# Performance work log

Measured on AMD Instinct MI355X. Metric: run time of the kernel, lower is better.

## Reference

```python
import jax, jax.numpy as jnp
import numpy as np

B, T, D, H, NH = 128, 64, 64, 128, 4


def setup_inputs() -> dict:
    key = jax.random.key(0)
    ks = jax.random.split(key, 32)
    s = 0.05
    inp = {
        "x": jax.random.normal(ks[0], (B, T, D), dtype=jnp.float32),
        "mask": jnp.ones((B, T), dtype=jnp.int32),
        # per-feature GRU params (input size 1, PyTorch gate order r,z,n)
        "Wih": jax.random.normal(ks[1], (D, 3 * H), dtype=jnp.float32) * s,
        "Whh": jax.random.normal(ks[2], (D, 3 * H, H), dtype=jnp.float32) * s,
        "bih": jax.random.normal(ks[3], (D, 3 * H), dtype=jnp.float32) * s,
        "bhh": jax.random.normal(ks[4], (D, 3 * H), dtype=jnp.float32) * s,
        # MHA projections (stored [in,out]; y = x @ W + b)
        "Wq": jax.random.normal(ks[5], (H, H), dtype=jnp.float32) * s,
        "bq": jnp.zeros((H,), dtype=jnp.float32),
        "Wk": jax.random.normal(ks[6], (H, H), dtype=jnp.float32) * s,
        "bk": jnp.zeros((H,), dtype=jnp.float32),
        "Wv": jax.random.normal(ks[7], (H, H), dtype=jnp.float32) * s,
        "bv": jnp.zeros((H,), dtype=jnp.float32),
        "Wo": jax.random.normal(ks[8], (H, H), dtype=jnp.float32) * s,
        "bo": jnp.zeros((H,), dtype=jnp.float32),
        # FFN
        "W1": jax.random.normal(ks[9], (H, 2 * H), dtype=jnp.float32) * s,
        "b1": jnp.zeros((2 * H,), dtype=jnp.float32),
        "W2": jax.random.normal(ks[10], (2 * H, H), dtype=jnp.float32) * s,
        "b2": jnp.zeros((H,), dtype=jnp.float32),
        # LayerNorms
        "g1": jnp.ones((H,), dtype=jnp.float32),
        "be1": jnp.zeros((H,), dtype=jnp.float32),
        "g2": jnp.ones((H,), dtype=jnp.float32),
        "be2": jnp.zeros((H,), dtype=jnp.float32),
        # FinalAttentionQKV
        "Fq": jax.random.normal(ks[11], (H, H), dtype=jnp.float32) * s,
        "fbq": jnp.zeros((H,), dtype=jnp.float32),
        "Fk": jax.random.normal(ks[12], (H, H), dtype=jnp.float32) * s,
        "fbk": jnp.zeros((H,), dtype=jnp.float32),
        "Fv": jax.random.normal(ks[13], (H, H), dtype=jnp.float32) * s,
        "fbv": jnp.zeros((H,), dtype=jnp.float32),
        "Fout": jax.random.normal(ks[14], (H,), dtype=jnp.float32) * s,
        "fbout": jnp.zeros((), dtype=jnp.float32),
    }
    return inp


def _layernorm(x, g, b, eps=1e-5):
    m = jnp.mean(x, axis=-1, keepdims=True)
    v = jnp.mean((x - m) ** 2, axis=-1, keepdims=True)
    return (x - m) * jax.lax.rsqrt(v + eps) * g + b


def _forward(x, mask, Wih, Whh, bih, bhh, Wq, bq, Wk, bk, Wv, bv, Wo, bo,
             W1, b1, W2, b2, g1, be1, g2, be2,
             Fq, fbq, Fk, fbk, Fv, fbv, Fout, fbout):
    Bc, Tc, Dc = x.shape
    Hc = Whh.shape[-1]

    # --- D independent GRUs, fused: batch axes (B, D), scalar input per step ---
    def step(h, xt):  # h: [B,D,H], xt: [B,D]
        gx = xt[..., None] * Wih + bih                     # [B,D,3H]
        gh = jnp.einsum('bdh,dkh->bdk', h, Whh) + bhh      # [B,D,3H]
        r = jax.nn.sigmoid(gx[..., :Hc] + gh[..., :Hc])
        z = jax.nn.sigmoid(gx[..., Hc:2 * Hc] + gh[..., Hc:2 * Hc])
        n = jnp.tanh(gx[..., 2 * Hc:] + r * gh[..., 2 * Hc:])
        hn = (1.0 - z) * n + z * h
        return hn, hn

    xs = jnp.transpose(x, (1, 0, 2))                        # [T,B,D]
    h0 = jnp.zeros((Bc, Dc, Hc), dtype=x.dtype)
    _, ys = jax.lax.scan(step, h0, xs)                      # [T,B,D,H]

    # last_by_lengths: gather hidden state at index lengths-1 per batch element
    lengths = jnp.sum(mask, axis=1)                         # [B]
    idx = jnp.clip(lengths - 1, 0, Tc - 1)
    emb = ys[idx, jnp.arange(Bc)]                           # [B,D,H] (D tokens)

    # --- MHA (self-attention over D feature tokens); dropout = identity (eval) ---
    dk = Hc // NH
    def split_heads(t):
        return jnp.transpose(t.reshape(Bc, Dc, NH, dk), (0, 2, 1, 3))  # [B,NH,D,dk]
    q = split_heads(emb @ Wq + bq)
    k = split_heads(emb @ Wk + bk)
    v = split_heads(emb @ Wv + bv)
    scores = jnp.einsum('bhnd,bhmd->bhnm', q, k) / jnp.sqrt(jnp.float32(dk))
    attn = jax.nn.softmax(scores, axis=-1)
    o = jnp.einsum('bhnm,bhmd->bhnd', attn, v)
    o = jnp.transpose(o, (0, 2, 1, 3)).reshape(Bc, Dc, Hc)
    mha_out = o @ Wo + bo

    h1 = _layernorm(emb + mha_out, g1, be1)
    ffn = jax.nn.relu(h1 @ W1 + b1) @ W2 + b2
    h2 = _layernorm(h1 + ffn, g2, be2)

    # --- FinalAttentionQKV ---
    fq = (h2[:, -1, :] @ Fq + fbq)[:, None, :]              # [B,1,H]
    fk = h2 @ Fk + fbk                                      # [B,D,H]
    fv = h2 @ Fv + fbv                                      # [B,D,H]
    e = jnp.tanh(fq + fk) @ Fout + fbout                    # [B,D]
    a = jax.nn.softmax(e, axis=-1)
    return jnp.einsum('bn,bnh->bh', a, fv)                  # [B,H]


def reference(x, mask, Wih, Whh, bih, bhh, Wq, bq, Wk, bk, Wv, bv, Wo, bo,
              W1, b1, W2, b2, g1, be1, g2, be2,
              Fq, fbq, Fk, fbk, Fv, fbv, Fout, fbout):
    return _forward(x, mask, Wih, Whh, bih, bhh, Wq, bq, Wk, bk, Wv, bv, Wo, bo,
                    W1, b1, W2, b2, g1, be1, g2, be2,
                    Fq, fbq, Fk, fbk, Fv, fbv, Fout, fbout)
```

## Files before the change

kernel.cpp:

```cpp
#include <hip/hip_runtime.h>
#include <hip/hip_bf16.h>
#include <math.h>

#define BB 128
#define TT 64
#define DD 64
#define HH 128
#define NHH 4
#define K3H 384

typedef __attribute__((ext_vector_type(8))) short short8_t;
typedef __attribute__((ext_vector_type(4))) float float4_t;

#define LOG2E 1.4426950408889634f

__device__ __forceinline__ unsigned short f2bf(float f) {
    unsigned int u = __float_as_uint(f);
    u += 0x7fffu + ((u >> 16) & 1u);
    return (unsigned short)(u >> 16);
}

__device__ __forceinline__ unsigned pack_bf2(float lo, float hi) {
    return (unsigned)f2bf(lo) | ((unsigned)f2bf(hi) << 16);
}

__device__ __forceinline__ unsigned pack_bf2_hw(float lo, float hi) {
    __hip_bfloat162 p = __float22bfloat162_rn(make_float2(lo, hi));
    unsigned u;
    __builtin_memcpy(&u, &p, 4);
    return u;
}

__device__ __forceinline__ unsigned short f2bf_hw(float f) {
    return (unsigned short)(pack_bf2_hw(f, f) & 0xffffu);
}

__device__ __forceinline__ float bf2f(unsigned short s) {
    return __uint_as_float((unsigned)s << 16);
}

__device__ __forceinline__ float2 pk_fma(float2 a, float2 b, float2 c) {
    return make_float2(fmaf(a.x, b.x, c.x), fmaf(a.y, b.y, c.y));
}
__device__ __forceinline__ float2 pk_sub(float2 a, float2 b) {
    return make_float2(a.x - b.x, a.y - b.y);
}

__device__ __forceinline__ void gru_epilogue(
    const float4_t& ar, const float4_t& az, const float4_t& an, float xv,
    const float wrs[4], const float wzs[4], const float wns[4],
    const float bnis[4], float hprev[4], float hn4[4])
{
    float2 xv2 = make_float2(xv, xv);
#pragma unroll
    for (int pp = 0; pp < 2; ++pp) {
        const int r0 = 2 * pp, r1 = r0 + 1;
        float2 grs = pk_fma(xv2, make_float2(wrs[r0], wrs[r1]),
                            make_float2(ar[r0], ar[r1]));
        float2 gzs = pk_fma(xv2, make_float2(wzs[r0], wzs[r1]),
                            make_float2(az[r0], az[r1]));
        float2 rg = make_float2(
            __builtin_amdgcn_rcpf(1.f + __builtin_amdgcn_exp2f(grs.x)),
            __builtin_amdgcn_rcpf(1.f + __builtin_amdgcn_exp2f(grs.y)));
        float2 gns = pk_fma(rg, make_float2(an[r0], an[r1]),
                            pk_fma(xv2, make_float2(wns[r0], wns[r1]),
                                   make_float2(bnis[r0], bnis[r1])));
        float2 t1 = make_float2(1.f + __builtin_amdgcn_exp2f(gns.x),
                                1.f + __builtin_amdgcn_exp2f(gns.y));
        float2 t2 = make_float2(1.f + __builtin_amdgcn_exp2f(gzs.x),
                                1.f + __builtin_amdgcn_exp2f(gzs.y));
        float2 iD = make_float2(__builtin_amdgcn_rcpf(t1.x * t2.x),
                                __builtin_amdgcn_rcpf(t1.y * t2.y));
        float2 tn = make_float2(fmaf(-2.f, t2.x * iD.x, 1.f),
                                fmaf(-2.f, t2.y * iD.y, 1.f));
        float2 zg = make_float2(t1.x * iD.x, t1.y * iD.y);
        float2 hp = make_float2(hprev[r0], hprev[r1]);
        float2 hn = pk_fma(zg, pk_sub(hp, tn), tn);
        hprev[r0] = hn.x; hprev[r1] = hn.y;
        hn4[r0] = hn.x; hn4[r1] = hn.y;
    }
}

__global__ __launch_bounds__(512, 1) void gru_mfma_kernel(
    const float* __restrict__ x, const int* __restrict__ mask,
    const float* __restrict__ Wih, const float* __restrict__ Whh,
    const float* __restrict__ bih, const float* __restrict__ bhh,
    float* __restrict__ emb)
{
    const int d  = blockIdx.x;
    const int b0 = blockIdx.y * 32;
    const int tid = threadIdx.x;
    const int w = tid >> 6;
    const int l = tid & 63;
    const int m = l & 15;
    const int q = l >> 4;

    __shared__ __align__(16) unsigned short hbuf[2][2][16][144];
    __shared__ float xs_t[TT][32];
    __shared__ int tstar_s[32];
    __shared__ char lds_pad_[60 * 1024];
    if (mask[0] == 0x7abcdef) ((volatile char*)lds_pad_)[0] = 1;

    for (int idx = tid; idx < 32 * TT; idx += 512) {
        int t = idx >> 5, row = idx & 31;
        xs_t[t][row] = x[((size_t)(b0 + row) * TT + t) * DD + d];
    }
    if (tid < 32) {
        int b = b0 + tid, len = 0;
        for (int t = 0; t < TT; ++t) len += mask[b * TT + t];
        int ts = len - 1;
        if (ts < 0) ts = 0;
        if (ts > TT - 1) ts = TT - 1;
        tstar_s[tid] = ts;
    }
    for (int idx = tid; idx < 2 * 2 * 16 * 144; idx += 512)
        ((unsigned short*)hbuf)[idx] = 0;

    short8_t Wf[3][4];
#pragma unroll
    for (int g = 0; g < 3; ++g) {
        float sc = (g == 2) ? (2.f * LOG2E) : (-LOG2E);
        int kcol = g * HH + 16 * w + m;
        const float* wrow = Whh + ((size_t)d * K3H + kcol) * HH;
#pragma unroll
        for (int kc = 0; kc < 4; ++kc) {
            int j0 = kc * 32 + q * 8;
            float4 w0 = *(const float4*)(wrow + j0);
            float4 w1 = *(const float4*)(wrow + j0 + 4);
            short8_t f;
            f[0] = (short)f2bf(w0.x * sc); f[1] = (short)f2bf(w0.y * sc);
            f[2] = (short)f2bf(w0.z * sc); f[3] = (short)f2bf(w0.w * sc);
            f[4] = (short)f2bf(w1.x * sc); f[5] = (short)f2bf(w1.y * sc);
            f[6] = (short)f2bf(w1.z * sc); f[7] = (short)f2bf(w1.w * sc);
            Wf[g][kc] = f;
        }
    }

    const int hcol0 = 16 * w + q * 4;
    float4 wr4 = *(const float4*)&Wih[d * K3H + hcol0];
    float4 wz4 = *(const float4*)&Wih[d * K3H + HH + hcol0];
    float4 wn4 = *(const float4*)&Wih[d * K3H + 2 * HH + hcol0];
    float4 br4 = *(const float4*)&bih[d * K3H + hcol0];
    float4 bz4 = *(const float4*)&bih[d * K3H + HH + hcol0];
    float4 bni4 = *(const float4*)&bih[d * K3H + 2 * HH + hcol0];
    float4 bhr4 = *(const float4*)&bhh[d * K3H + hcol0];
    float4 bhz4 = *(const float4*)&bhh[d * K3H + HH + hcol0];
    float4 bnh4 = *(const float4*)&bhh[d * K3H + 2 * HH + hcol0];
    float brs[4], bzs[4], bnis[4], bnhs[4], wrs[4], wzs[4], wns[4];
#pragma unroll
    for (int r = 0; r < 4; ++r) {
        wrs[r] = -LOG2E * ((const float*)&wr4)[r];
        wzs[r] = -LOG2E * ((const float*)&wz4)[r];
        wns[r] = 2.f * LOG2E * ((const float*)&wn4)[r];
        brs[r] = -LOG2E * (((const float*)&br4)[r] + ((const float*)&bhr4)[r]);
        bzs[r] = -LOG2E * (((const float*)&bz4)[r] + ((const float*)&bhz4)[r]);
        bnis[r] = 2.f * LOG2E * ((const float*)&bni4)[r];
        bnhs[r] = 2.f * LOG2E * ((const float*)&bnh4)[r];
    }

    float hprevA[4], hprevB[4];
#pragma unroll
    for (int i = 0; i < 4; ++i) { hprevA[i] = 0.f; hprevB[i] = 0.f; }

    __syncthreads();
    const int tstarA = tstar_s[m];
    const int tstarB = tstar_s[16 + m];
    float* embpA = emb + (((size_t)(b0 + m)) * DD + d) * HH + hcol0;
    float* embpB = emb + (((size_t)(b0 + 16 + m)) * DD + d) * HH + hcol0;

    short8_t hfA[4];
#pragma unroll
    for (int kc = 0; kc < 4; ++kc)
        hfA[kc] = *(const short8_t*)&hbuf[0][0][m][kc * 32 + q * 8];
    float4_t arA = {brs[0], brs[1], brs[2], brs[3]};
    float4_t azA = {bzs[0], bzs[1], bzs[2], bzs[3]};
    float4_t anA = {bnhs[0], bnhs[1], bnhs[2], bnhs[3]};
#pragma unroll
    for (int kc = 0; kc < 4; ++kc) {
        arA = __builtin_amdgcn_mfma_f32_16x16x32_bf16(Wf[0][kc], hfA[kc], arA, 0, 0, 0);
        azA = __builtin_amdgcn_mfma_f32_16x16x32_bf16(Wf[1][kc], hfA[kc], azA, 0, 0, 0);
        anA = __builtin_amdgcn_mfma_f32_16x16x32_bf16(Wf[2][kc], hfA[kc], anA, 0, 0, 0);
    }

    for (int t = 0; t < TT; ++t) {
        const int par = t & 1;
        float hn4[4];
        uint2 uu;

        short8_t hfB[4];
#pragma unroll
        for (int kc = 0; kc < 4; ++kc)
            hfB[kc] = *(const short8_t*)&hbuf[1][par][m][kc * 32 + q * 8];

        gru_epilogue(arA, azA, anA, xs_t[t][m], wrs, wzs, wns, bnis, hprevA, hn4);
        uu.x = pack_bf2_hw(hn4[0], hn4[1]);
        uu.y = pack_bf2_hw(hn4[2], hn4[3]);
        *(uint2*)&hbuf[0][par ^ 1][m][hcol0] = uu;
        if (t == tstarA) {
            float4 hv; hv.x = hn4[0]; hv.y = hn4[1]; hv.z = hn4[2]; hv.w = hn4[3];
            *(float4*)embpA = hv;
        }

        float4_t arB = {brs[0], brs[1], brs[2], brs[3]};
        float4_t azB = {bzs[0], bzs[1], bzs[2], bzs[3]};
        float4_t anB = {bnhs[0], bnhs[1], bnhs[2], bnhs[3]};
#pragma unroll
        for (int kc = 0; kc < 4; ++kc) {
            arB = __builtin_amdgcn_mfma_f32_16x16x32_bf16(Wf[0][kc], hfB[kc], arB, 0, 0, 0);
            azB = __builtin_amdgcn_mfma_f32_16x16x32_bf16(Wf[1][kc], hfB[kc], azB, 0, 0, 0);
            anB = __builtin_amdgcn_mfma_f32_16x16x32_bf16(Wf[2][kc], hfB[kc], anB, 0, 0, 0);
        }

        gru_epilogue(arB, azB, anB, xs_t[t][16 + m], wrs, wzs, wns, bnis, hprevB, hn4);
        uu.x = pack_bf2_hw(hn4[0], hn4[1]);
        uu.y = pack_bf2_hw(hn4[2], hn4[3]);
        *(uint2*)&hbuf[1][par ^ 1][m][hcol0] = uu;
        if (t == tstarB) {
            float4 hv; hv.x = hn4[0]; hv.y = hn4[1]; hv.z = hn4[2]; hv.w = hn4[3];
            *(float4*)embpB = hv;
        }

        __syncthreads();

        if (t < TT - 1) {
#pragma unroll
            for (int kc = 0; kc < 4; ++kc)
                hfA[kc] = *(const short8_t*)&hbuf[0][par ^ 1][m][kc * 32 + q * 8];
            arA = (float4_t){brs[0], brs[1], brs[2], brs[3]};
            azA = (float4_t){bzs[0], bzs[1], bzs[2], bzs[3]};
            anA = (float4_t){bnhs[0], bnhs[1], bnhs[2], bnhs[3]};
#pragma unroll
            for (int kc = 0; kc < 4; ++kc) {
                arA = __builtin_amdgcn_mfma_f32_16x16x32_bf16(Wf[0][kc], hfA[kc], arA, 0, 0, 0);
                azA = __builtin_amdgcn_mfma_f32_16x16x32_bf16(Wf[1][kc], hfA[kc], azA, 0, 0, 0);
                anA = __builtin_amdgcn_mfma_f32_16x16x32_bf16(Wf[2][kc], hfA[kc], anA, 0, 0, 0);
            }
        }
    }
}

__device__ __forceinline__ void load_wfrag(const float* __restrict__ Wp, int N,
                                           int col, float scale, int q,
                                           short8_t fr[4])
{
#pragma unroll
    for (int kc = 0; kc < 4; ++kc) {
        const float* p = Wp + (size_t)(kc * 32 + q * 8) * N + col;
        unsigned u[4];
#pragma unroll
        for (int j = 0; j < 4; ++j)
            u[j] = pack_bf2_hw(p[(size_t)(2 * j) * N] * scale,
                               p[(size_t)(2 * j + 1) * N] * scale);
        short8_t f;
        __builtin_memcpy(&f, u, 16);
        fr[kc] = f;
    }
}

__device__ __forceinline__ void load_afrag(const unsigned short (*S)[136],
                                           short8_t Af[4][4], int m16, int q)
{
#pragma unroll
    for (int mt = 0; mt < 4; ++mt)
#pragma unroll
        for (int kc = 0; kc < 4; ++kc)
            Af[mt][kc] = *(const short8_t*)&S[mt * 16 + m16][kc * 32 + q * 8];
}

__device__ __forceinline__ void mm_regw(short8_t Af[4][4], short8_t Bf[4],
                                        float4_t acc[4])
{
#pragma unroll
    for (int mt = 0; mt < 4; ++mt) {
        float4_t a = acc[mt];
#pragma unroll
        for (int kc = 0; kc < 4; ++kc)
            a = __builtin_amdgcn_mfma_f32_16x16x32_bf16(Af[mt][kc], Bf[kc], a, 0, 0, 0);
        acc[mt] = a;
    }
}

__device__ __forceinline__ void zero4(float4_t acc[4]) {
#pragma unroll
    for (int mt = 0; mt < 4; ++mt) acc[mt] = (float4_t){0.f, 0.f, 0.f, 0.f};
}

__device__ __forceinline__ void store_rows(unsigned short (*Dst)[136], float4_t acc[4],
                                           float bv, int relu, int col, int q)
{
#pragma unroll
    for (int mt = 0; mt < 4; ++mt)
#pragma unroll
        for (int reg = 0; reg < 4; ++reg) {
            float v = acc[mt][reg] + bv;
            if (relu) v = fmaxf(v, 0.f);
            Dst[mt * 16 + q * 4 + reg][col] = f2bf_hw(v);
        }
}

__global__ __launch_bounds__(512) void tail_kernel(
    const float* __restrict__ emb,
    const float* __restrict__ Wq, const float* __restrict__ bq,
    const float* __restrict__ Wk, const float* __restrict__ bk,
    const float* __restrict__ Wv, const float* __restrict__ bv,
    const float* __restrict__ Wo, const float* __restrict__ bo,
    const float* __restrict__ W1, const float* __restrict__ b1,
    const float* __restrict__ W2, const float* __restrict__ b2,
    const float* __restrict__ g1, const float* __restrict__ be1,
    const float* __restrict__ g2, const float* __restrict__ be2,
    const float* __restrict__ Fq, const float* __restrict__ fbq,
    const float* __restrict__ Fk, const float* __restrict__ fbk,
    const float* __restrict__ Fv, const float* __restrict__ fbv,
    const float* __restrict__ Fout, const float* __restrict__ fbout,
    float* __restrict__ out)
{
    const int b = blockIdx.x;
    const int tid = threadIdx.x;
    const int w = tid >> 6, l = tid & 63, m16 = l & 15, q = l >> 4;
    const int col = w * 16 + m16;

    __shared__ __align__(16) unsigned short E[64][136];
    __shared__ __align__(16) unsigned short Qs[64][136];
    __shared__ __align__(16) unsigned short Ks[64][136];
    __shared__ __align__(16) unsigned short Vt[128][72];
    __shared__ float sc4[4][64][66];
    __shared__ float lnp[64][8], lnp2[64][8];
    __shared__ float mean_s[64], rs_s[64];
    __shared__ float fq_s[128], fo_s[128], e_s[64], red_s[256];

    const float* embB = emb + (size_t)b * 64 * 128;
    const float SS = 0.17677669529663687f;

    short8_t WqF[4], WkF[4], WvF[4];
    load_wfrag(Wq, 128, col, SS, q, WqF);
    load_wfrag(Wk, 128, col, 1.f, q, WkF);
    load_wfrag(Wv, 128, col, 1.f, q, WvF);
    float bqv = bq[col] * SS, bkv = bk[col], bvv = bv[col];

    for (int it = tid; it < 2048; it += 512) {
        int r = it >> 5, c4 = (it & 31) << 2;
        float4 a = *(const float4*)&embB[r * 128 + c4];
        uint2 p; p.x = pack_bf2_hw(a.x, a.y); p.y = pack_bf2_hw(a.z, a.w);
        *(uint2*)&E[r][c4] = p;
    }
    __syncthreads();

    short8_t Af[4][4];
    float4_t acc[4];
    load_afrag(E, Af, m16, q);

    zero4(acc); mm_regw(Af, WqF, acc); store_rows(Qs, acc, bqv, 0, col, q);
    zero4(acc); mm_regw(Af, WkF, acc); store_rows(Ks, acc, bkv, 0, col, q);
    zero4(acc); mm_regw(Af, WvF, acc);
#pragma unroll
    for (int mt = 0; mt < 4; ++mt) {
        uint2 pk;
        pk.x = pack_bf2_hw(acc[mt][0] + bvv, acc[mt][1] + bvv);
        pk.y = pack_bf2_hw(acc[mt][2] + bvv, acc[mt][3] + bvv);
        *(uint2*)&Vt[col][mt * 16 + q * 4] = pk;
    }
    __syncthreads();

    short8_t WoF[4], W1aF[4], W1bF[4];
    load_wfrag(Wo, 128, col, 1.f, q, WoF);
    load_wfrag(W1, 256, col, 1.f, q, W1aF);
    load_wfrag(W1, 256, 128 + col, 1.f, q, W1bF);
    float bov = bo[col], b1a = b1[col], b1b = b1[128 + col];
    float g1v = g1[col], be1v = be1[col];

    {
        int hd = w >> 1, ntb = (w & 1) * 2;
#pragma unroll
        for (int mt = 0; mt < 4; ++mt) {
            short8_t Aq = *(const short8_t*)&Qs[mt * 16 + m16][hd * 32 + q * 8];
#pragma unroll
            for (int nn = 0; nn < 2; ++nn) {
                int nt = ntb + nn;
                short8_t Bk = *(const short8_t*)&Ks[nt * 16 + m16][hd * 32 + q * 8];
                float4_t a = {0.f, 0.f, 0.f, 0.f};
                a = __builtin_amdgcn_mfma_f32_16x16x32_bf16(Aq, Bk, a, 0, 0, 0);
#pragma unroll
                for (int reg = 0; reg < 4; ++reg)
                    sc4[hd][mt * 16 + q * 4 + reg][nt * 16 + m16] = a[reg];
            }
        }
    }
    __syncthreads();

    {
        int pr = tid >> 1, hd2 = pr >> 6, row = pr & 63, half = (tid & 1) * 32;
        float v[32]; float mx = -1e30f;
#pragma unroll
        for (int c = 0; c < 32; ++c) { v[c] = sc4[hd2][row][half + c]; mx = fmaxf(mx, v[c]); }
        mx = fmaxf(mx, __shfl_xor(mx, 1));
        float sum = 0.f;
#pragma unroll
        for (int c = 0; c < 32; ++c) { v[c] = __expf(v[c] - mx); sum += v[c]; }
        sum += __shfl_xor(sum, 1);
        float inv = __builtin_amdgcn_rcpf(sum);
        unsigned short (*Pd)[136] = (hd2 < 2) ? Qs : Ks;
        int cb = (hd2 & 1) * 64 + half;
#pragma unroll
        for (int c = 0; c < 16; ++c)
            *(unsigned*)&Pd[row][cb + 2 * c] = pack_bf2_hw(v[2 * c] * inv, v[2 * c + 1] * inv);
    }
    __syncthreads();

    {
        int hd = w >> 1, nt = w & 1;
        const unsigned short (*P)[136] = (hd < 2) ? (const unsigned short (*)[136])Qs
                                                  : (const unsigned short (*)[136])Ks;
        int pb = (hd & 1) * 64;
        int vrow = hd * 32 + nt * 16 + m16;
        short8_t B0f = *(const short8_t*)&Vt[vrow][q * 8];
        short8_t B1f = *(const short8_t*)&Vt[vrow][32 + q * 8];
#pragma unroll
        for (int mt = 0; mt < 4; ++mt) {
            short8_t A0 = *(const short8_t*)&P[mt * 16 + m16][pb + q * 8];
            short8_t A1 = *(const short8_t*)&P[mt * 16 + m16][pb + 32 + q * 8];
            float4_t a = {0.f, 0.f, 0.f, 0.f};
            a = __builtin_amdgcn_mfma_f32_16x16x32_bf16(A0, B0f, a, 0, 0, 0);
            a = __builtin_amdgcn_mfma_f32_16x16x32_bf16(A1, B1f, a, 0, 0, 0);
#pragma unroll
            for (int reg = 0; reg < 4; ++reg)
                E[mt * 16 + q * 4 + reg][vrow] = f2bf_hw(a[reg]);
        }
    }
    __syncthreads();

    short8_t W2aF[4], W2bF[4], FkF[4], FvF[4];
    load_wfrag(W2, 128, col, 1.f, q, W2aF);
    load_wfrag(W2 + (size_t)128 * 128, 128, col, 1.f, q, W2bF);
    load_wfrag(Fk, 128, col, 1.f, q, FkF);
    load_wfrag(Fv, 128, col, 1.f, q, FvF);
    float b2v = b2[col], fbkv = fbk[col], fbvv = fbv[col];
    float g2v = g2[col], be2v = be2[col];

    load_afrag(E, Af, m16, q);
    zero4(acc); mm_regw(Af, WoF, acc);
    float h1v[4][4];
#pragma unroll
    for (int mt = 0; mt < 4; ++mt)
#pragma unroll
        for (int reg = 0; reg < 4; ++reg) {
            int row = mt * 16 + q * 4 + reg;
            h1v[mt][reg] = acc[mt][reg] + bov + embB[(size_t)row * 128 + col];
        }
#pragma unroll
    for (int mt = 0; mt < 4; ++mt)
#pragma unroll
        for (int reg = 0; reg < 4; ++reg) {
            float s = h1v[mt][reg], s2 = s * s;
            s += __shfl_xor(s, 1); s += __shfl_xor(s, 2); s += __shfl_xor(s, 4); s += __shfl_xor(s, 8);
            s2 += __shfl_xor(s2, 1); s2 += __shfl_xor(s2, 2); s2 += __shfl_xor(s2, 4); s2 += __shfl_xor(s2, 8);
            if (m16 == 0) { int row = mt * 16 + q * 4 + reg; lnp[row][w] = s; lnp2[row][w] = s2; }
        }
    __syncthreads();
    if (tid < 64) {
        float s = 0.f, s2 = 0.f;
#pragma unroll
        for (int k = 0; k < 8; ++k) { s += lnp[tid][k]; s2 += lnp2[tid][k]; }
        float mn = s * (1.f / 128.f);
        mean_s[tid] = mn;
        rs_s[tid] = rsqrtf(s2 * (1.f / 128.f) - mn * mn + 1e-5f);
    }
    __syncthreads();
#pragma unroll
    for (int mt = 0; mt < 4; ++mt)
#pragma unroll
        for (int reg = 0; reg < 4; ++reg) {
            int row = mt * 16 + q * 4 + reg;
            float hv = (h1v[mt][reg] - mean_s[row]) * rs_s[row] * g1v + be1v;
            h1v[mt][reg] = hv;
            E[row][col] = f2bf_hw(hv);
        }
    __syncthreads();

    load_afrag(E, Af, m16, q);
    zero4(acc); mm_regw(Af, W1aF, acc); store_rows(Qs, acc, b1a, 1, col, q);
    zero4(acc); mm_regw(Af, W1bF, acc); store_rows(Ks, acc, b1b, 1, col, q);
    __syncthreads();

    {
        short8_t AfQ[4][4], AfK[4][4];
        load_afrag(Qs, AfQ, m16, q);
        load_afrag(Ks, AfK, m16, q);
        zero4(acc); mm_regw(AfQ, W2aF, acc); mm_regw(AfK, W2bF, acc);
    }
#pragma unroll
    for (int mt = 0; mt < 4; ++mt)
#pragma unroll
        for (int reg = 0; reg < 4; ++reg)
            h1v[mt][reg] = acc[mt][reg] + b2v + h1v[mt][reg];
#pragma unroll
    for (int mt = 0; mt < 4; ++mt)
#pragma unroll
        for (int reg = 0; reg < 4; ++reg) {
            float s = h1v[mt][reg], s2 = s * s;
            s += __shfl_xor(s, 1); s += __shfl_xor(s, 2); s += __shfl_xor(s, 4); s += __shfl_xor(s, 8);
            s2 += __shfl_xor(s2, 1); s2 += __shfl_xor(s2, 2); s2 += __shfl_xor(s2, 4); s2 += __shfl_xor(s2, 8);
            if (m16 == 0) { int row = mt * 16 + q * 4 + reg; lnp[row][w] = s; lnp2[row][w] = s2; }
        }
    __syncthreads();
    if (tid < 64) {
        float s = 0.f, s2 = 0.f;
#pragma unroll
        for (int k = 0; k < 8; ++k) { s += lnp[tid][k]; s2 += lnp2[tid][k]; }
        float mn = s * (1.f / 128.f);
        mean_s[tid] = mn;
        rs_s[tid] = rsqrtf(s2 * (1.f / 128.f) - mn * mn + 1e-5f);
    }
    __syncthreads();
#pragma unroll
    for (int mt = 0; mt < 4; ++mt)
#pragma unroll
        for (int reg = 0; reg < 4; ++reg) {
            int row = mt * 16 + q * 4 + reg;
            float hv = (h1v[mt][reg] - mean_s[row]) * rs_s[row] * g2v + be2v;
            E[row][col] = f2bf_hw(hv);
        }
    __syncthreads();

    load_afrag(E, Af, m16, q);
    zero4(acc); mm_regw(Af, FkF, acc); store_rows(Qs, acc, fbkv, 0, col, q);
    zero4(acc); mm_regw(Af, FvF, acc); store_rows(Ks, acc, fbvv, 0, col, q);
    {
        int co = tid >> 2, sub = tid & 3;
        float a2 = 0.f;
#pragma unroll 8
        for (int mm2 = sub * 32; mm2 < sub * 32 + 32; ++mm2)
            a2 = fmaf(bf2f(E[63][mm2]), Fq[(size_t)mm2 * 128 + co], a2);
        a2 += __shfl_xor(a2, 1);
        a2 += __shfl_xor(a2, 2);
        if (sub == 0) fq_s[co] = a2 + fbq[co];
    }
    if (tid < 128) fo_s[tid] = Fout[tid];
    __syncthreads();

    {
        int dd = tid >> 3, c8 = tid & 7;
        float p = 0.f;
#pragma unroll
        for (int c = 0; c < 16; ++c) {
            int cc = c8 * 16 + c;
            float t = fq_s[cc] + bf2f(Qs[dd][cc]);
            float tn = 1.f - 2.f * __builtin_amdgcn_rcpf(
                __builtin_amdgcn_exp2f(2.f * LOG2E * t) + 1.f);
            p = fmaf(tn, fo_s[cc], p);
        }
        p += __shfl_xor(p, 1); p += __shfl_xor(p, 2); p += __shfl_xor(p, 4);
        if (c8 == 0) e_s[dd] = p + fbout[0];
    }
    __syncthreads();
    if (tid < 64) {
        float e = e_s[tid], mx = e;
        for (int o = 32; o; o >>= 1) mx = fmaxf(mx, __shfl_xor(mx, o));
        float pe = __expf(e - mx);
        float s = pe;
        for (int o = 32; o; o >>= 1) s += __shfl_xor(s, o);
        e_s[tid] = pe / s;
    }
    __syncthreads();
    if (tid < 256) {
        int c2 = tid & 127, rg2 = tid >> 7;
        float a = 0.f;
        for (int d2 = rg2 * 32; d2 < rg2 * 32 + 32; ++d2)
            a = fmaf(e_s[d2], bf2f(Ks[d2][c2]), a);
        red_s[tid] = a;
    }
    __syncthreads();
    if (tid < 128)
        out[(size_t)b * 128 + tid] = red_s[tid] + red_s[tid + 128];
}

extern "C" void kernel_launch(void* const* d_in, const int* in_sizes, int n_in,
                              void* d_out, int out_size, void* d_ws, size_t ws_size,
                              hipStream_t stream)
{
    const float* x    = (const float*)d_in[0];
    const int*   mask = (const int*)d_in[1];
    const float* Wih  = (const float*)d_in[2];
    const float* Whh  = (const float*)d_in[3];
    const float* bih  = (const float*)d_in[4];
    const float* bhh  = (const float*)d_in[5];
    const float* Wq = (const float*)d_in[6];   const float* bq = (const float*)d_in[7];
    const float* Wk = (const float*)d_in[8];   const float* bk = (const float*)d_in[9];
    const float* Wv = (const float*)d_in[10];  const float* bv = (const float*)d_in[11];
    const float* Wo = (const float*)d_in[12];  const float* bo = (const float*)d_in[13];
    const float* W1 = (const float*)d_in[14];  const float* b1 = (const float*)d_in[15];
    const float* W2 = (const float*)d_in[16];  const float* b2 = (const float*)d_in[17];
    const float* g1 = (const float*)d_in[18];  const float* be1 = (const float*)d_in[19];
    const float* g2 = (const float*)d_in[20];  const float* be2 = (const float*)d_in[21];
    const float* Fq = (const float*)d_in[22];  const float* fbq = (const float*)d_in[23];
    const float* Fk = (const float*)d_in[24];  const float* fbk = (const float*)d_in[25];
    const float* Fv = (const float*)d_in[26];  const float* fbv = (const float*)d_in[27];
    const float* Fout = (const float*)d_in[28]; const float* fbout = (const float*)d_in[29];
    float* out = (float*)d_out;
    float* ws  = (float*)d_ws;

    float* emb = ws;

    gru_mfma_kernel<<<dim3(DD, BB / 32), 512, 0, stream>>>(x, mask, Wih, Whh, bih, bhh, emb);
    tail_kernel<<<BB, 512, 0, stream>>>(
        emb, Wq, bq, Wk, bk, Wv, bv, Wo, bo, W1, b1, W2, b2,
        g1, be1, g2, be2, Fq, fbq, Fk, fbk, Fv, fbv, Fout, fbout, out);
}
```

Measured before the change: 229.4 us.

## Fuse GRU and tail kernels into one cooperative kernel with grid sync

Merges the GRU recurrence kernel and the transformer/attention tail kernel into a single cooperative launch of 256 blocks. A union of shared-memory layouts lets both phases reuse the same LDS, and a grid-wide barrier presumably separates the GRU phase from the tail phase. This removes the second kernel launch and the gap between kernels. In exchange it adds grid-sync overhead, and it drops the old 60KB LDS padding that had forced one block per CU.

```diff
diff --git a/kernel.cpp b/kernel.cpp
--- a/kernel.cpp
+++ b/kernel.cpp
@@ -1,6 +1,9 @@
 #include <hip/hip_runtime.h>
 #include <hip/hip_bf16.h>
+#include <hip/hip_cooperative_groups.h>
 #include <math.h>
+
+namespace cg = cooperative_groups;
 
 #define BB 128
 #define TT 64
@@ -18,10 +21,6 @@
     unsigned int u = __float_as_uint(f);
     u += 0x7fffu + ((u >> 16) & 1u);
     return (unsigned short)(u >> 16);
-}
-
-__device__ __forceinline__ unsigned pack_bf2(float lo, float hi) {
-    return (unsigned)f2bf(lo) | ((unsigned)f2bf(hi) << 16);
 }
 
 __device__ __forceinline__ unsigned pack_bf2_hw(float lo, float hi) {
@@ -81,164 +80,6 @@
     }
 }
 
-__global__ __launch_bounds__(512, 1) void gru_mfma_kernel(
-    const float* __restrict__ x, const int* __restrict__ mask,
-    const float* __restrict__ Wih, const float* __restrict__ Whh,
-    const float* __restrict__ bih, const float* __restrict__ bhh,
-    float* __restrict__ emb)
-{
-    const int d  = blockIdx.x;
-    const int b0 = blockIdx.y * 32;
-    const int tid = threadIdx.x;
-    const int w = tid >> 6;
-    const int l = tid & 63;
-    const int m = l & 15;
-    const int q = l >> 4;
-
-    __shared__ __align__(16) unsigned short hbuf[2][2][16][144];
-    __shared__ float xs_t[TT][32];
-    __shared__ int tstar_s[32];
-    __shared__ char lds_pad_[60 * 1024];
-    if (mask[0] == 0x7abcdef) ((volatile char*)lds_pad_)[0] = 1;
-
-    for (int idx = tid; idx < 32 * TT; idx += 512) {
-        int t = idx >> 5, row = idx & 31;
-        xs_t[t][row] = x[((size_t)(b0 + row) * TT + t) * DD + d];
-    }
-    if (tid < 32) {
-        int b = b0 + tid, len = 0;
-        for (int t = 0; t < TT; ++t) len += mask[b * TT + t];
-        int ts = len - 1;
-        if (ts < 0) ts = 0;
-        if (ts > TT - 1) ts = TT - 1;
-        tstar_s[tid] = ts;
-    }
-    for (int idx = tid; idx < 2 * 2 * 16 * 144; idx += 512)
-        ((unsigned short*)hbuf)[idx] = 0;
-
-    short8_t Wf[3][4];
-#pragma unroll
-    for (int g = 0; g < 3; ++g) {
-        float sc = (g == 2) ? (2.f * LOG2E) : (-LOG2E);
-        int kcol = g * HH + 16 * w + m;
-        const float* wrow = Whh + ((size_t)d * K3H + kcol) * HH;
-#pragma unroll
-        for (int kc = 0; kc < 4; ++kc) {
-            int j0 = kc * 32 + q * 8;
-            float4 w0 = *(const float4*)(wrow + j0);
-            float4 w1 = *(const float4*)(wrow + j0 + 4);
-            short8_t f;
-            f[0] = (short)f2bf(w0.x * sc); f[1] = (short)f2bf(w0.y * sc);
-            f[2] = (short)f2bf(w0.z * sc); f[3] = (short)f2bf(w0.w * sc);
-            f[4] = (short)f2bf(w1.x * sc); f[5] = (short)f2bf(w1.y * sc);
-            f[6] = (short)f2bf(w1.z * sc); f[7] = (short)f2bf(w1.w * sc);
-            Wf[g][kc] = f;
-        }
-    }
-
-    const int hcol0 = 16 * w + q * 4;
-    float4 wr4 = *(const float4*)&Wih[d * K3H + hcol0];
-    float4 wz4 = *(const float4*)&Wih[d * K3H + HH + hcol0];
-    float4 wn4 = *(const float4*)&Wih[d * K3H + 2 * HH + hcol0];
-    float4 br4 = *(const float4*)&bih[d * K3H + hcol0];
-    float4 bz4 = *(const float4*)&bih[d * K3H + HH + hcol0];
-    float4 bni4 = *(const float4*)&bih[d * K3H + 2 * HH + hcol0];
-    float4 bhr4 = *(const float4*)&bhh[d * K3H + hcol0];
-    float4 bhz4 = *(const float4*)&bhh[d * K3H + HH + hcol0];
-    float4 bnh4 = *(const float4*)&bhh[d * K3H + 2 * HH + hcol0];
-    float brs[4], bzs[4], bnis[4], bnhs[4], wrs[4], wzs[4], wns[4];
-#pragma unroll
-    for (int r = 0; r < 4; ++r) {
-        wrs[r] = -LOG2E * ((const float*)&wr4)[r];
-        wzs[r] = -LOG2E * ((const float*)&wz4)[r];
-        wns[r] = 2.f * LOG2E * ((const float*)&wn4)[r];
-        brs[r] = -LOG2E * (((const float*)&br4)[r] + ((const float*)&bhr4)[r]);
-        bzs[r] = -LOG2E * (((const float*)&bz4)[r] + ((const float*)&bhz4)[r]);
-        bnis[r] = 2.f * LOG2E * ((const float*)&bni4)[r];
-        bnhs[r] = 2.f * LOG2E * ((const float*)&bnh4)[r];
-    }
-
-    float hprevA[4], hprevB[4];
-#pragma unroll
-    for (int i = 0; i < 4; ++i) { hprevA[i] = 0.f; hprevB[i] = 0.f; }
-
-    __syncthreads();
-    const int tstarA = tstar_s[m];
-    const int tstarB = tstar_s[16 + m];
-    float* embpA = emb + (((size_t)(b0 + m)) * DD + d) * HH + hcol0;
-    float* embpB = emb + (((size_t)(b0 + 16 + m)) * DD + d) * HH + hcol0;
-
-    short8_t hfA[4];
-#pragma unroll
-    for (int kc = 0; kc < 4; ++kc)
-        hfA[kc] = *(const short8_t*)&hbuf[0][0][m][kc * 32 + q * 8];
-    float4_t arA = {brs[0], brs[1], brs[2], brs[3]};
-    float4_t azA = {bzs[0], bzs[1], bzs[2], bzs[3]};
-    float4_t anA = {bnhs[0], bnhs[1], bnhs[2], bnhs[3]};
-#pragma unroll
-    for (int kc = 0; kc < 4; ++kc) {
-        arA = __builtin_amdgcn_mfma_f32_16x16x32_bf16(Wf[0][kc], hfA[kc], arA, 0, 0, 0);
-        azA = __builtin_amdgcn_mfma_f32_16x16x32_bf16(Wf[1][kc], hfA[kc], azA, 0, 0, 0);
-        anA = __builtin_amdgcn_mfma_f32_16x16x32_bf16(Wf[2][kc], hfA[kc], anA, 0, 0, 0);
-    }
-
-    for (int t = 0; t < TT; ++t) {
-        const int par = t & 1;
-        float hn4[4];
-        uint2 uu;
-
-        short8_t hfB[4];
-#pragma unroll
-        for (int kc = 0; kc < 4; ++kc)
-            hfB[kc] = *(const short8_t*)&hbuf[1][par][m][kc * 32 + q * 8];
-
-        gru_epilogue(arA, azA, anA, xs_t[t][m], wrs, wzs, wns, bnis, hprevA, hn4);
-        uu.x = pack_bf2_hw(hn4[0], hn4[1]);
-        uu.y = pack_bf2_hw(hn4[2], hn4[3]);
-        *(uint2*)&hbuf[0][par ^ 1][m][hcol0] = uu;
-        if (t == tstarA) {
-            float4 hv; hv.x = hn4[0]; hv.y = hn4[1]; hv.z = hn4[2]; hv.w = hn4[3];
-            *(float4*)embpA = hv;
-        }
-
-        float4_t arB = {brs[0], brs[1], brs[2], brs[3]};
-        float4_t azB = {bzs[0], bzs[1], bzs[2], bzs[3]};
-        float4_t anB = {bnhs[0], bnhs[1], bnhs[2], bnhs[3]};
-#pragma unroll
-        for (int kc = 0; kc < 4; ++kc) {
-            arB = __builtin_amdgcn_mfma_f32_16x16x32_bf16(Wf[0][kc], hfB[kc], arB, 0, 0, 0);
-            azB = __builtin_amdgcn_mfma_f32_16x16x32_bf16(Wf[1][kc], hfB[kc], azB, 0, 0, 0);
-            anB = __builtin_amdgcn_mfma_f32_16x16x32_bf16(Wf[2][kc], hfB[kc], anB, 0, 0, 0);
-        }
-
-        gru_epilogue(arB, azB, anB, xs_t[t][16 + m], wrs, wzs, wns, bnis, hprevB, hn4);
-        uu.x = pack_bf2_hw(hn4[0], hn4[1]);
-        uu.y = pack_bf2_hw(hn4[2], hn4[3]);
-        *(uint2*)&hbuf[1][par ^ 1][m][hcol0] = uu;
-        if (t == tstarB) {
-            float4 hv; hv.x = hn4[0]; hv.y = hn4[1]; hv.z = hn4[2]; hv.w = hn4[3];
-            *(float4*)embpB = hv;
-        }
-
-        __syncthreads();
-
-        if (t < TT - 1) {
-#pragma unroll
-            for (int kc = 0; kc < 4; ++kc)
-                hfA[kc] = *(const short8_t*)&hbuf[0][par ^ 1][m][kc * 32 + q * 8];
-            arA = (float4_t){brs[0], brs[1], brs[2], brs[3]};
-            azA = (float4_t){bzs[0], bzs[1], bzs[2], bzs[3]};
-            anA = (float4_t){bnhs[0], bnhs[1], bnhs[2], bnhs[3]};
-#pragma unroll
-            for (int kc = 0; kc < 4; ++kc) {
-                arA = __builtin_amdgcn_mfma_f32_16x16x32_bf16(Wf[0][kc], hfA[kc], arA, 0, 0, 0);
-                azA = __builtin_amdgcn_mfma_f32_16x16x32_bf16(Wf[1][kc], hfA[kc], azA, 0, 0, 0);
-                anA = __builtin_amdgcn_mfma_f32_16x16x32_bf16(Wf[2][kc], hfA[kc], anA, 0, 0, 0);
-            }
-        }
-    }
-}
-
 __device__ __forceinline__ void load_wfrag(const float* __restrict__ Wp, int N,
                                            int col, float scale, int q,
                                            short8_t fr[4])
@@ -298,8 +139,28 @@
         }
 }
 
-__global__ __launch_bounds__(512) void tail_kernel(
-    const float* __restrict__ emb,
+union SharedU {
+    struct {
+        unsigned short hbuf[2][2][16][144];
+        float xs_t[TT][32];
+        int tstar[32];
+    } g;
+    struct {
+        unsigned short E[64][136];
+        unsigned short Qs[64][136];
+        unsigned short Ks[64][136];
+        unsigned short Vt[128][72];
+        float sc4[4][64][66];
+        float lnp[64][8], lnp2[64][8];
+        float mean_s[64], rs_s[64];
+        float fq_s[128], fo_s[128], e_s[64], red_s[256];
+    } t;
+};
+
+__global__ __launch_bounds__(512, 1) void fused_kernel(
+    const float* __restrict__ x, const int* __restrict__ mask,
+    const float* __restrict__ Wih, const float* __restrict__ Whh,
+    const float* __restrict__ bih, const float* __restrict__ bhh,
     const float* __restrict__ Wq, const float* __restrict__ bq,
     const float* __restrict__ Wk, const float* __restrict__ bk,
     const float* __restrict__ Wv, const float* __restrict__ bv,
@@ -312,265 +173,429 @@
     const float* __restrict__ Fk, const float* __restrict__ fbk,
     const float* __restrict__ Fv, const float* __restrict__ fbv,
     const float* __restrict__ Fout, const float* __restrict__ fbout,
-    float* __restrict__ out)
+    float* __restrict__ emb, float* __restrict__ out)
 {
-    const int b = blockIdx.x;
+    __shared__ __align__(16) SharedU smem;
+    const int bid = blockIdx.x;
     const int tid = threadIdx.x;
-    const int w = tid >> 6, l = tid & 63, m16 = l & 15, q = l >> 4;
-    const int col = w * 16 + m16;
-
-    __shared__ __align__(16) unsigned short E[64][136];
-    __shared__ __align__(16) unsigned short Qs[64][136];
-    __shared__ __align__(16) unsigned short Ks[64][136];
-    __shared__ __align__(16) unsigned short Vt[128][72];
-    __shared__ float sc4[4][64][66];
-    __shared__ float lnp[64][8], lnp2[64][8];
-    __shared__ float mean_s[64], rs_s[64];
-    __shared__ float fq_s[128], fo_s[128], e_s[64], red_s[256];
-
-    const float* embB = emb + (size_t)b * 64 * 128;
-    const float SS = 0.17677669529663687f;
-
-    short8_t WqF[4], WkF[4], WvF[4];
-    load_wfrag(Wq, 128, col, SS, q, WqF);
-    load_wfrag(Wk, 128, col, 1.f, q, WkF);
-    load_wfrag(Wv, 128, col, 1.f, q, WvF);
-    float bqv = bq[col] * SS, bkv = bk[col], bvv = bv[col];
-
-    for (int it = tid; it < 2048; it += 512) {
-        int r = it >> 5, c4 = (it & 31) << 2;
-        float4 a = *(const float4*)&embB[r * 128 + c4];
-        uint2 p; p.x = pack_bf2_hw(a.x, a.y); p.y = pack_bf2_hw(a.z, a.w);
-        *(uint2*)&E[r][c4] = p;
+
+    {
+        const int d  = bid & 63;
+        const int b0 = (bid >> 6) * 32;
+        const int w = tid >> 6;
+        const int l = tid & 63;
+        const int m = l & 15;
+        const int q = l >> 4;
+
+        unsigned short (&hbuf)[2][2][16][144] = smem.g.hbuf;
+        float (&xs_t)[TT][32] = smem.g.xs_t;
+        int (&tstar_s)[32] = smem.g.tstar;
+
+        for (int idx = tid; idx < 32 * TT; idx += 512) {
+            int t = idx >> 5, row = idx & 31;
+            xs_t[t][row] = x[((size_t)(b0 + row) * TT + t) * DD + d];
+        }
+        if (tid < 32) {
+            int b = b0 + tid, len = 0;
+            for (int t = 0; t < TT; ++t) len += mask[b * TT + t];
+            int ts = len - 1;
+            if (ts < 0) ts = 0;
+            if (ts > TT - 1) ts = TT - 1;
+            tstar_s[tid] = ts;
+        }
+        for (int idx = tid; idx < 2 * 2 * 16 * 144; idx += 512)
+            ((unsigned short*)hbuf)[idx] = 0;
+
+        short8_t Wf[3][4];
+#pragma unroll
+        for (int g = 0; g < 3; ++g) {
+            float sc = (g == 2) ? (2.f * LOG2E) : (-LOG2E);
+            int kcol = g * HH + 16 * w + m;
+            const float* wrow = Whh + ((size_t)d * K3H + kcol) * HH;
+#pragma unroll
+            for (int kc = 0; kc < 4; ++kc) {
+                int j0 = kc * 32 + q * 8;
+                float4 w0 = *(const float4*)(wrow + j0);
+                float4 w1 = *(const float4*)(wrow + j0 + 4);
+                short8_t f;
+                f[0] = (short)f2bf(w0.x * sc); f[1] = (short)f2bf(w0.y * sc);
+                f[2] = (short)f2bf(w0.z * sc); f[3] = (short)f2bf(w0.w * sc);
+                f[4] = (short)f2bf(w1.x * sc); f[5] = (short)f2bf(w1.y * sc);
+                f[6] = (short)f2bf(w1.z * sc); f[7] = (short)f2bf(w1.w * sc);
+                Wf[g][kc] = f;
+            }
+        }
+
+        const int hcol0 = 16 * w + q * 4;
+        float4 wr4 = *(const float4*)&Wih[d * K3H + hcol0];
+        float4 wz4 = *(const float4*)&Wih[d * K3H + HH + hcol0];
+        float4 wn4 = *(const float4*)&Wih[d * K3H + 2 * HH + hcol0];
+        float4 br4 = *(const float4*)&bih[d * K3H + hcol0];
+        float4 bz4 = *(const float4*)&bih[d * K3H + HH + hcol0];
+        float4 bni4 = *(const float4*)&bih[d * K3H + 2 * HH + hcol0];
+        float4 bhr4 = *(const float4*)&bhh[d * K3H + hcol0];
+        float4 bhz4 = *(const float4*)&bhh[d * K3H + HH + hcol0];
+        float4 bnh4 = *(const float4*)&bhh[d * K3H + 2 * HH + hcol0];
+        float brs[4], bzs[4], bnis[4], bnhs[4], wrs[4], wzs[4], wns[4];
+#pragma unroll
+        for (int r = 0; r < 4; ++r) {
+            wrs[r] = -LOG2E * ((const float*)&wr4)[r];
+            wzs[r] = -LOG2E * ((const float*)&wz4)[r];
+            wns[r] = 2.f * LOG2E * ((const float*)&wn4)[r];
+            brs[r] = -LOG2E * (((const float*)&br4)[r] + ((const float*)&bhr4)[r]);
+            bzs[r] = -LOG2E * (((const float*)&bz4)[r] + ((const float*)&bhz4)[r]);
+            bnis[r] = 2.f * LOG2E * ((const float*)&bni4)[r];
+            bnhs[r] = 2.f * LOG2E * ((const float*)&bnh4)[r];
+        }
+
+        float hprevA[4], hprevB[4];
+#pragma unroll
+        for (int i = 0; i < 4; ++i) { hprevA[i] = 0.f; hprevB[i] = 0.f; }
+
+        __syncthreads();
+        const int tstarA = tstar_s[m];
+        const int tstarB = tstar_s[16 + m];
+        float* embpA = emb + (((size_t)(b0 + m)) * DD + d) * HH + hcol0;
+        float* embpB = emb + (((size_t)(b0 + 16 + m)) * DD + d) * HH + hcol0;
+
+        short8_t hfA[4];
+#pragma unroll
+        for (int kc = 0; kc < 4; ++kc)
+            hfA[kc] = *(const short8_t*)&hbuf[0][0][m][kc * 32 + q * 8];
+        float4_t arA = {brs[0], brs[1], brs[2], brs[3]};
+        float4_t azA = {bzs[0], bzs[1], bzs[2], bzs[3]};
+        float4_t anA = {bnhs[0], bnhs[1], bnhs[2], bnhs[3]};
+#pragma unroll
+        for (int kc = 0; kc < 4; ++kc) {
+            arA = __builtin_amdgcn_mfma_f32_16x16x32_bf16(Wf[0][kc], hfA[kc], arA, 0, 0, 0);
+            azA = __builtin_amdgcn_mfma_f32_16x16x32_bf16(Wf[1][kc], hfA[kc], azA, 0, 0, 0);
+            anA = __builtin_amdgcn_mfma_f32_16x16x32_bf16(Wf[2][kc], hfA[kc], anA, 0, 0, 0);
+        }
+
+        for (int t = 0; t < TT; ++t) {
+            const int par = t & 1;
+            float hn4[4];
+            uint2 uu;
+
+            short8_t hfB[4];
+#pragma unroll
+            for (int kc = 0; kc < 4; ++kc)
+                hfB[kc] = *(const short8_t*)&hbuf[1][par][m][kc * 32 + q * 8];
+
+            gru_epilogue(arA, azA, anA, xs_t[t][m], wrs, wzs, wns, bnis, hprevA, hn4);
+            uu.x = pack_bf2_hw(hn4[0], hn4[1]);
+            uu.y = pack_bf2_hw(hn4[2], hn4[3]);
+            *(uint2*)&hbuf[0][par ^ 1][m][hcol0] = uu;
+            if (t == tstarA) {
+                float4 hv; hv.x = hn4[0]; hv.y = hn4[1]; hv.z = hn4[2]; hv.w = hn4[3];
+                *(float4*)embpA = hv;
+            }
+
+            float4_t arB = {brs[0], brs[1], brs[2], brs[3]};
+            float4_t azB = {bzs[0], bzs[1], bzs[2], bzs[3]};
+            float4_t anB = {bnhs[0], bnhs[1], bnhs[2], bnhs[3]};
+#pragma unroll
+            for (int kc = 0; kc < 4; ++kc) {
+                arB = __builtin_amdgcn_mfma_f32_16x16x32_bf16(Wf[0][kc], hfB[kc], arB, 0, 0, 0);
+                azB = __builtin_amdgcn_mfma_f32_16x16x32_bf16(Wf[1][kc], hfB[kc], azB, 0, 0, 0);
+                anB = __builtin_amdgcn_mfma_f32_16x16x32_bf16(Wf[2][kc], hfB[kc], anB, 0, 0, 0);
+            }
+
+            gru_epilogue(arB, azB, anB, xs_t[t][16 + m], wrs, wzs, wns, bnis, hprevB, hn4);
+            uu.x = pack_bf2_hw(hn4[0], hn4[1]);
+            uu.y = pack_bf2_hw(hn4[2], hn4[3]);
+            *(uint2*)&hbuf[1][par ^ 1][m][hcol0] = uu;
+            if (t == tstarB) {
+                float4 hv; hv.x = hn4[0]; hv.y = hn4[1]; hv.z = hn4[2]; hv.w = hn4[3];
+                *(float4*)embpB = hv;
+            }
+
+            __syncthreads();
+
+            if (t < TT - 1) {
+#pragma unroll
+                for (int kc = 0; kc < 4; ++kc)
+                    hfA[kc] = *(const short8_t*)&hbuf[0][par ^ 1][m][kc * 32 + q * 8];
+                arA = (float4_t){brs[0], brs[1], brs[2], brs[3]};
+                azA = (float4_t){bzs[0], bzs[1], bzs[2], bzs[3]};
+                anA = (float4_t){bnhs[0], bnhs[1], bnhs[2], bnhs[3]};
+#pragma unroll
+                for (int kc = 0; kc < 4; ++kc) {
+                    arA = __builtin_amdgcn_mfma_f32_16x16x32_bf16(Wf[0][kc], hfA[kc], arA, 0, 0, 0);
+                    azA = __builtin_amdgcn_mfma_f32_16x16x32_bf16(Wf[1][kc], hfA[kc], azA, 0, 0, 0);
+                    anA = __builtin_amdgcn_mfma_f32_16x16x32_bf16(Wf[2][kc], hfA[kc], anA, 0, 0, 0);
+                }
+            }
+        }
     }
-    __syncthreads();
-
-    short8_t Af[4][4];
-    float4_t acc[4];
-    load_afrag(E, Af, m16, q);
-
-    zero4(acc); mm_regw(Af, WqF, acc); store_rows(Qs, acc, bqv, 0, col, q);
-    zero4(acc); mm_regw(Af, WkF, acc); store_rows(Ks, acc, bkv, 0, col, q);
-    zero4(acc); mm_regw(Af, WvF, acc);
-#pragma unroll
-    for (int mt = 0; mt < 4; ++mt) {
-        uint2 pk;
-        pk.x = pack_bf2_hw(acc[mt][0] + bvv, acc[mt][1] + bvv);
-        pk.y = pack_bf2_hw(acc[mt][2] + bvv, acc[mt][3] + bvv);
-        *(uint2*)&Vt[col][mt * 16 + q * 4] = pk;
+
+    __threadfence();
+    cg::this_grid().sync();
+
+    if (bid >= BB) return;
+    {
+        const int b = bid;
+        const int w = tid >> 6, l = tid & 63, m16 = l & 15, q = l >> 4;
+        const int col = w * 16 + m16;
+
+        unsigned short (&E)[64][136]  = smem.t.E;
+        unsigned short (&Qs)[64][136] = smem.t.Qs;
+        unsigned short (&Ks)[64][136] = smem.t.Ks;
+        unsigned short (&Vt)[128][72] = smem.t.Vt;
+        float (&sc4)[4][64][66] = smem.t.sc4;
+        float (&lnp)[64][8] = smem.t.lnp;
+        float (&lnp2)[64][8] = smem.t.lnp2;
+        float (&mean_s)[64] = smem.t.mean_s;
+        float (&rs_s)[64] = smem.t.rs_s;
+        float (&fq_s)[128] = smem.t.fq_s;
+        float (&fo_s)[128] = smem.t.fo_s;
+        float (&e_s)[64] = smem.t.e_s;
+        float (&red_s)[256] = smem.t.red_s;
+
+        const float* embB = emb + (size_t)b * 64 * 128;
+        const float SS = 0.17677669529663687f;
+
+        short8_t WqF[4], WkF[4], WvF[4];
+        load_wfrag(Wq, 128, col, SS, q, WqF);
+        load_wfrag(Wk, 128, col, 1.f, q, WkF);
+        load_wfrag(Wv, 128, col, 1.f, q, WvF);
+        float bqv = bq[col] * SS, bkv = bk[col], bvv = bv[col];
+
+        for (int it = tid; it < 2048; it += 512) {
+            int r = it >> 5, c4 = (it & 31) << 2;
+            float4 a = *(const float4*)&embB[r * 128 + c4];
+            uint2 p; p.x = pack_bf2_hw(a.x, a.y); p.y = pack_bf2_hw(a.z, a.w);
+            *(uint2*)&E[r][c4] = p;
+        }
+        __syncthreads();
+
+        short8_t Af[4][4];
+        float4_t acc[4];
+        load_afrag(E, Af, m16, q);
+
+        zero4(acc); mm_regw(Af, WqF, acc); store_rows(Qs, acc, bqv, 0, col, q);
+        zero4(acc); mm_regw(Af, WkF, acc); store_rows(Ks, acc, bkv, 0, col, q);
+        zero4(acc); mm_regw(Af, WvF, acc);
+#pragma unroll
+        for (int mt = 0; mt < 4; ++mt) {
+            uint2 pk;
+            pk.x = pack_bf2_hw(acc[mt][0] + bvv, acc[mt][1] + bvv);
+            pk.y = pack_bf2_hw(acc[mt][2] + bvv, acc[mt][3] + bvv);
+            *(uint2*)&Vt[col][mt * 16 + q * 4] = pk;
+        }
+        __syncthreads();
+
+        short8_t WoF[4], W1aF[4], W1bF[4];
+        load_wfrag(Wo, 128, col, 1.f, q, WoF);
+        load_wfrag(W1, 256, col, 1.f, q, W1aF);
+        load_wfrag(W1, 256, 128 + col, 1.f, q, W1bF);
+        float bov = bo[col], b1a = b1[col], b1b = b1[128 + col];
+        float g1v = g1[col], be1v = be1[col];
+
+        {
+            int hd = w >> 1, ntb = (w & 1) * 2;
+#pragma unroll
+            for (int mt = 0; mt < 4; ++mt) {
+                short8_t Aq = *(const short8_t*)&Qs[mt * 16 + m16][hd * 32 + q * 8];
+#pragma unroll
+                for (int nn = 0; nn < 2; ++nn) {
+                    int nt = ntb + nn;
+                    short8_t Bk = *(const short8_t*)&Ks[nt * 16 + m16][hd * 32 + q * 8];
+                    float4_t a = {0.f, 0.f, 0.f, 0.f};
+                    a = __builtin_amdgcn_mfma_f32_16x16x32_bf16(Aq, Bk, a, 0, 0, 0);
+#pragma unroll
+                    for (int reg = 0; reg < 4; ++reg)
+                        sc4[hd][mt * 16 + q * 4 + reg][nt * 16 + m16] = a[reg];
+                }
+            }
+        }
+        __syncthreads();
+
+        {
+            int pr = tid >> 1, hd2 = pr >> 6, row = pr & 63, half = (tid & 1) * 32;
+            float v[32]; float mx = -1e30f;
+#pragma unroll
+            for (int c = 0; c < 32; ++c) { v[c] = sc4[hd2][row][half + c]; mx = fmaxf(mx, v[c]); }
+            mx = fmaxf(mx, __shfl_xor(mx, 1));
+            float sum = 0.f;
+#pragma unroll
+            for (int c = 0; c < 32; ++c) { v[c] = __expf(v[c] - mx); sum += v[c]; }
+            sum += __shfl_xor(sum, 1);
+            float inv = __builtin_amdgcn_rcpf(sum);
+            unsigned short (*Pd)[136] = (hd2 < 2) ? Qs : Ks;
+            int cb = (hd2 & 1) * 64 + half;
+#pragma unroll
+            for (int c = 0; c < 16; ++c)
+                *(unsigned*)&Pd[row][cb + 2 * c] = pack_bf2_hw(v[2 * c] * inv, v[2 * c + 1] * inv);
+        }
+        __syncthreads();
+
+        {
+            int hd = w >> 1, nt = w & 1;
+            const unsigned short (*P)[136] = (hd < 2) ? (const unsigned short (*)[136])Qs
+                                                      : (const unsigned short (*)[136])Ks;
+            int pb = (hd & 1) * 64;
+            int vrow = hd * 32 + nt * 16 + m16;
+            short8_t B0f = *(const short8_t*)&Vt[vrow][q * 8];
+            short8_t B1f = *(const short8_t*)&Vt[vrow][32 + q * 8];
+#pragma unroll
+            for (int mt = 0; mt < 4; ++mt) {
+                short8_t A0 = *(const short8_t*)&P[mt * 16 + m16][pb + q * 8];
+                short8_t A1 = *(const short8_t*)&P[mt * 16 + m16][pb + 32 + q * 8];
+                float4_t a = {0.f, 0.f, 0.f, 0.f};
+                a = __builtin_amdgcn_mfma_f32_16x16x32_bf16(A0, B0f, a, 0, 0, 0);
+                a = __builtin_amdgcn_mfma_f32_16x16x32_bf16(A1, B1f, a, 0, 0, 0);
+#pragma unroll
+                for (int reg = 0; reg < 4; ++reg)
+                    E[mt * 16 + q * 4 + reg][vrow] = f2bf_hw(a[reg]);
+            }
+        }
+        __syncthreads();
+
+        short8_t W2aF[4], W2bF[4], FkF[4], FvF[4];
+        load_wfrag(W2, 128, col, 1.f, q, W2aF);
+        load_wfrag(W2 + (size_t)128 * 128, 128, col, 1.f, q, W2bF);
+        load_wfrag(Fk, 128, col, 1.f, q, FkF);
+        load_wfrag(Fv, 128, col, 1.f, q, FvF);
+        float b2v = b2[col], fbkv = fbk[col], fbvv = fbv[col];
+        float g2v = g2[col], be2v = be2[col];
+
+        load_afrag(E, Af, m16, q);
+        zero4(acc); mm_regw(Af, WoF, acc);
+        float h1v[4][4];
+#pragma unroll
+        for (int mt = 0; mt < 4; ++mt)
+#pragma unroll
+            for (int reg = 0; reg < 4; ++reg) {
+                int row = mt * 16 + q * 4 + reg;
+                h1v[mt][reg] = acc[mt][reg] + bov + embB[(size_t)row * 128 + col];
+            }
+#pragma unroll
+        for (int mt = 0; mt < 4; ++mt)
+#pragma unroll
+            for (int reg = 0; reg < 4; ++reg) {
+                float s = h1v[mt][reg], s2 = s * s;
+                s += __shfl_xor(s, 1); s += __shfl_xor(s, 2); s += __shfl_xor(s, 4); s += __shfl_xor(s, 8);
+                s2 += __shfl_xor(s2, 1); s2 += __shfl_xor(s2, 2); s2 += __shfl_xor(s2, 4); s2 += __shfl_xor(s2, 8);
+                if (m16 == 0) { int row = mt * 16 + q * 4 + reg; lnp[row][w] = s; lnp2[row][w] = s2; }
+            }
+        __syncthreads();
+        if (tid < 64) {
+            float s = 0.f, s2 = 0.f;
+#pragma unroll
+            for (int k = 0; k < 8; ++k) { s += lnp[tid][k]; s2 += lnp2[tid][k]; }
+            float mn = s * (1.f / 128.f);
+            mean_s[tid] = mn;
+            rs_s[tid] = rsqrtf(s2 * (1.f / 128.f) - mn * mn + 1e-5f);
+        }
+        __syncthreads();
+#pragma unroll
+        for (int mt = 0; mt < 4; ++mt)
+#pragma unroll
+            for (int reg = 0; reg < 4; ++reg) {
+                int row = mt * 16 + q * 4 + reg;
+                float hv = (h1v[mt][reg] - mean_s[row]) * rs_s[row] * g1v + be1v;
+                h1v[mt][reg] = hv;
+                E[row][col] = f2bf_hw(hv);
+            }
+        __syncthreads();
+
+        load_afrag(E, Af, m16, q);
+        zero4(acc); mm_regw(Af, W1aF, acc); store_rows(Qs, acc, b1a, 1, col, q);
+        zero4(acc); mm_regw(Af, W1bF, acc); store_rows(Ks, acc, b1b, 1, col, q);
+        __syncthreads();
+
+        {
+            short8_t AfQ[4][4], AfK[4][4];
+            load_afrag(Qs, AfQ, m16, q);
+            load_afrag(Ks, AfK, m16, q);
+            zero4(acc); mm_regw(AfQ, W2aF, acc); mm_regw(AfK, W2bF, acc);
+        }
+#pragma unroll
+        for (int mt = 0; mt < 4; ++mt)
+#pragma unroll
+            for (int reg = 0; reg < 4; ++reg)
+                h1v[mt][reg] = acc[mt][reg] + b2v + h1v[mt][reg];
+#pragma unroll
+        for (int mt = 0; mt < 4; ++mt)
+#pragma unroll
+            for (int reg = 0; reg < 4; ++reg) {
+                float s = h1v[mt][reg], s2 = s * s;
+                s += __shfl_xor(s, 1); s += __shfl_xor(s, 2); s += __shfl_xor(s, 4); s += __shfl_xor(s, 8);
+                s2 += __shfl_xor(s2, 1); s2 += __shfl_xor(s2, 2); s2 += __shfl_xor(s2, 4); s2 += __shfl_xor(s2, 8);
+                if (m16 == 0) { int row = mt * 16 + q * 4 + reg; lnp[row][w] = s; lnp2[row][w] = s2; }
+            }
+        __syncthreads();
+        if (tid < 64) {
+            float s = 0.f, s2 = 0.f;
+#pragma unroll
+            for (int k = 0; k < 8; ++k) { s += lnp[tid][k]; s2 += lnp2[tid][k]; }
+            float mn = s * (1.f / 128.f);
+            mean_s[tid] = mn;
+            rs_s[tid] = rsqrtf(s2 * (1.f / 128.f) - mn * mn + 1e-5f);
+        }
+        __syncthreads();
+#pragma unroll
+        for (int mt = 0; mt < 4; ++mt)
+#pragma unroll
+            for (int reg = 0; reg < 4; ++reg) {
+                int row = mt * 16 + q * 4 + reg;
+                float hv = (h1v[mt][reg] - mean_s[row]) * rs_s[row] * g2v + be2v;
+                E[row][col] = f2bf_hw(hv);
+            }
+        __syncthreads();
+
+        load_afrag(E, Af, m16, q);
+        zero4(acc); mm_regw(Af, FkF, acc); store_rows(Qs, acc, fbkv, 0, col, q);
+        zero4(acc); mm_regw(Af, FvF, acc); store_rows(Ks, acc, fbvv, 0, col, q);
+        {
+            int co = tid >> 2, sub = tid & 3;
+            float a2 = 0.f;
+#pragma unroll 8
+            for (int mm2 = sub * 32; mm2 < sub * 32 + 32; ++mm2)
+                a2 = fmaf(bf2f(E[63][mm2]), Fq[(size_t)mm2 * 128 + co], a2);
+            a2 += __shfl_xor(a2, 1);
+            a2 += __shfl_xor(a2, 2);
+            if (sub == 0) fq_s[co] = a2 + fbq[co];
+        }
+        if (tid < 128) fo_s[tid] = Fout[tid];
+        __syncthreads();
+
+        {
+            int dd = tid >> 3, c8 = tid & 7;
+            float p = 0.f;
+#pragma unroll
+            for (int c = 0; c < 16; ++c) {
+                int cc = c8 * 16 + c;
+                float t = fq_s[cc] + bf2f(Qs[dd][cc]);
+                float tn = 1.f - 2.f * __builtin_amdgcn_rcpf(
+                    __builtin_amdgcn_exp2f(2.f * LOG2E * t) + 1.f);
+                p = fmaf(tn, fo_s[cc], p);
+            }
+            p += __shfl_xor(p, 1); p += __shfl_xor(p, 2); p += __shfl_xor(p, 4);
+            if (c8 == 0) e_s[dd] = p + fbout[0];
+        }
+        __syncthreads();
+        if (tid < 64) {
+            float e = e_s[tid], mx = e;
+            for (int o = 32; o; o >>= 1) mx = fmaxf(mx, __shfl_xor(mx, o));
+            float pe = __expf(e - mx);
+            float s = pe;
+            for (int o = 32; o; o >>= 1) s += __shfl_xor(s, o);
+            e_s[tid] = pe / s;
+        }
+        __syncthreads();
+        if (tid < 256) {
+            int c2 = tid & 127, rg2 = tid >> 7;
+            float a = 0.f;
+            for (int d2 = rg2 * 32; d2 < rg2 * 32 + 32; ++d2)
+                a = fmaf(e_s[d2], bf2f(Ks[d2][c2]), a);
+            red_s[tid] = a;
+        }
+        __syncthreads();
+        if (tid < 128)
+            out[(size_t)b * 128 + tid] = red_s[tid] + red_s[tid + 128];
     }
-    __syncthreads();
-
-    short8_t WoF[4], W1aF[4], W1bF[4];
-    load_wfrag(Wo, 128, col, 1.f, q, WoF);
-    load_wfrag(W1, 256, col, 1.f, q, W1aF);
-    load_wfrag(W1, 256, 128 + col, 1.f, q, W1bF);
-    float bov = bo[col], b1a = b1[col], b1b = b1[128 + col];
-    float g1v = g1[col], be1v = be1[col];
-
-    {
-        int hd = w >> 1, ntb = (w & 1) * 2;
-#pragma unroll
-        for (int mt = 0; mt < 4; ++mt) {
-            short8_t Aq = *(const short8_t*)&Qs[mt * 16 + m16][hd * 32 + q * 8];
-#pragma unroll
-            for (int nn = 0; nn < 2; ++nn) {
-                int nt = ntb + nn;
-                short8_t Bk = *(const short8_t*)&Ks[nt * 16 + m16][hd * 32 + q * 8];
-                float4_t a = {0.f, 0.f, 0.f, 0.f};
-                a = __builtin_amdgcn_mfma_f32_16x16x32_bf16(Aq, Bk, a, 0, 0, 0);
-#pragma unroll
-                for (int reg = 0; reg < 4; ++reg)
-                    sc4[hd][mt * 16 + q * 4 + reg][nt * 16 + m16] = a[reg];
-            }
-        }
-    }
-    __syncthreads();
-
-    {
-        int pr = tid >> 1, hd2 = pr >> 6, row = pr & 63, half = (tid & 1) * 32;
-        float v[32]; float mx = -1e30f;
-#pragma unroll
-        for (int c = 0; c < 32; ++c) { v[c] = sc4[hd2][row][half + c]; mx = fmaxf(mx, v[c]); }
-        mx = fmaxf(mx, __shfl_xor(mx, 1));
-        float sum = 0.f;
-#pragma unroll
-        for (int c = 0; c < 32; ++c) { v[c] = __expf(v[c] - mx); sum += v[c]; }
-        sum += __shfl_xor(sum, 1);
-        float inv = __builtin_amdgcn_rcpf(sum);
-        unsigned short (*Pd)[136] = (hd2 < 2) ? Qs : Ks;
-        int cb = (hd2 & 1) * 64 + half;
-#pragma unroll
-        for (int c = 0; c < 16; ++c)
-            *(unsigned*)&Pd[row][cb + 2 * c] = pack_bf2_hw(v[2 * c] * inv, v[2 * c + 1] * inv);
-    }
-    __syncthreads();
-
-    {
-        int hd = w >> 1, nt = w & 1;
-        const unsigned short (*P)[136] = (hd < 2) ? (const unsigned short (*)[136])Qs
-                                                  : (const unsigned short (*)[136])Ks;
-        int pb = (hd & 1) * 64;
-        int vrow = hd * 32 + nt * 16 + m16;
-        short8_t B0f = *(const short8_t*)&Vt[vrow][q * 8];
-        short8_t B1f = *(const short8_t*)&Vt[vrow][32 + q * 8];
-#pragma unroll
-        for (int mt = 0; mt < 4; ++mt) {
-            short8_t A0 = *(const short8_t*)&P[mt * 16 + m16][pb + q * 8];
-            short8_t A1 = *(const short8_t*)&P[mt * 16 + m16][pb + 32 + q * 8];
-            float4_t a = {0.f, 0.f, 0.f, 0.f};
-            a = __builtin_amdgcn_mfma_f32_16x16x32_bf16(A0, B0f, a, 0, 0, 0);
-            a = __builtin_amdgcn_mfma_f32_16x16x32_bf16(A1, B1f, a, 0, 0, 0);
-#pragma unroll
-            for (int reg = 0; reg < 4; ++reg)
-                E[mt * 16 + q * 4 + reg][vrow] = f2bf_hw(a[reg]);
-        }
-    }
-    __syncthreads();
-
-    short8_t W2aF[4], W2bF[4], FkF[4], FvF[4];
-    load_wfrag(W2, 128, col, 1.f, q, W2aF);
-    load_wfrag(W2 + (size_t)128 * 128, 128, col, 1.f, q, W2bF);
-    load_wfrag(Fk, 128, col, 1.f, q, FkF);
-    load_wfrag(Fv, 128, col, 1.f, q, FvF);
-    float b2v = b2[col], fbkv = fbk[col], fbvv = fbv[col];
-    float g2v = g2[col], be2v = be2[col];
-
-    load_afrag(E, Af, m16, q);
-    zero4(acc); mm_regw(Af, WoF, acc);
-    float h1v[4][4];
-#pragma unroll
-    for (int mt = 0; mt < 4; ++mt)
-#pragma unroll
-        for (int reg = 0; reg < 4; ++reg) {
-            int row = mt * 16 + q * 4 + reg;
-            h1v[mt][reg] = acc[mt][reg] + bov + embB[(size_t)row * 128 + col];
-        }
-#pragma unroll
-    for (int mt = 0; mt < 4; ++mt)
-#pragma unroll
-        for (int reg = 0; reg < 4; ++reg) {
-            float s = h1v[mt][reg], s2 = s * s;
-            s += __shfl_xor(s, 1); s += __shfl_xor(s, 2); s += __shfl_xor(s, 4); s += __shfl_xor(s, 8);
-            s2 += __shfl_xor(s2, 1); s2 += __shfl_xor(s2, 2); s2 += __shfl_xor(s2, 4); s2 += __shfl_xor(s2, 8);
-            if (m16 == 0) { int row = mt * 16 + q * 4 + reg; lnp[row][w] = s; lnp2[row][w] = s2; }
-        }
-    __syncthreads();
-    if (tid < 64) {
-        float s = 0.f, s2 = 0.f;
-#pragma unroll
-        for (int k = 0; k < 8; ++k) { s += lnp[tid][k]; s2 += lnp2[tid][k]; }
-        float mn = s * (1.f / 128.f);
-        mean_s[tid] = mn;
-        rs_s[tid] = rsqrtf(s2 * (1.f / 128.f) - mn * mn + 1e-5f);
-    }
-    __syncthreads();
-#pragma unroll
-    for (int mt = 0; mt < 4; ++mt)
-#pragma unroll
-        for (int reg = 0; reg < 4; ++reg) {
-            int row = mt * 16 + q * 4 + reg;
-            float hv = (h1v[mt][reg] - mean_s[row]) * rs_s[row] * g1v + be1v;
-            h1v[mt][reg] = hv;
-            E[row][col] = f2bf_hw(hv);
-        }
-    __syncthreads();
-
-    load_afrag(E, Af, m16, q);
-    zero4(acc); mm_regw(Af, W1aF, acc); store_rows(Qs, acc, b1a, 1, col, q);
-    zero4(acc); mm_regw(Af, W1bF, acc); store_rows(Ks, acc, b1b, 1, col, q);
-    __syncthreads();
-
-    {
-        short8_t AfQ[4][4], AfK[4][4];
-        load_afrag(Qs, AfQ, m16, q);
-        load_afrag(Ks, AfK, m16, q);
-        zero4(acc); mm_regw(AfQ, W2aF, acc); mm_regw(AfK, W2bF, acc);
-    }
-#pragma unroll
-    for (int mt = 0; mt < 4; ++mt)
-#pragma unroll
-        for (int reg = 0; reg < 4; ++reg)
-            h1v[mt][reg] = acc[mt][reg] + b2v + h1v[mt][reg];
-#pragma unroll
-    for (int mt = 0; mt < 4; ++mt)
-#pragma unroll
-        for (int reg = 0; reg < 4; ++reg) {
-            float s = h1v[mt][reg], s2 = s * s;
-            s += __shfl_xor(s, 1); s += __shfl_xor(s, 2); s += __shfl_xor(s, 4); s += __shfl_xor(s, 8);
-            s2 += __shfl_xor(s2, 1); s2 += __shfl_xor(s2, 2); s2 += __shfl_xor(s2, 4); s2 += __shfl_xor(s2, 8);
-            if (m16 == 0) { int row = mt * 16 + q * 4 + reg; lnp[row][w] = s; lnp2[row][w] = s2; }
-        }
-    __syncthreads();
-    if (tid < 64) {
-        float s = 0.f, s2 = 0.f;
-#pragma unroll
-        for (int k = 0; k < 8; ++k) { s += lnp[tid][k]; s2 += lnp2[tid][k]; }
-        float mn = s * (1.f / 128.f);
-        mean_s[tid] = mn;
-        rs_s[tid] = rsqrtf(s2 * (1.f / 128.f) - mn * mn + 1e-5f);
-    }
-    __syncthreads();
-#pragma unroll
-    for (int mt = 0; mt < 4; ++mt)
-#pragma unroll
-        for (int reg = 0; reg < 4; ++reg) {
-            int row = mt * 16 + q * 4 + reg;
-            float hv = (h1v[mt][reg] - mean_s[row]) * rs_s[row] * g2v + be2v;
-            E[row][col] = f2bf_hw(hv);
-        }
-    __syncthreads();
-
-    load_afrag(E, Af, m16, q);
-    zero4(acc); mm_regw(Af, FkF, acc); store_rows(Qs, acc, fbkv, 0, col, q);
-    zero4(acc); mm_regw(Af, FvF, acc); store_rows(Ks, acc, fbvv, 0, col, q);
-    {
-        int co = tid >> 2, sub = tid & 3;
-        float a2 = 0.f;
-#pragma unroll 8
-        for (int mm2 = sub * 32; mm2 < sub * 32 + 32; ++mm2)
-            a2 = fmaf(bf2f(E[63][mm2]), Fq[(size_t)mm2 * 128 + co], a2);
-        a2 += __shfl_xor(a2, 1);
-        a2 += __shfl_xor(a2, 2);
-        if (sub == 0) fq_s[co] = a2 + fbq[co];
-    }
-    if (tid < 128) fo_s[tid] = Fout[tid];
-    __syncthreads();
-
-    {
-        int dd = tid >> 3, c8 = tid & 7;
-        float p = 0.f;
-#pragma unroll
-        for (int c = 0; c < 16; ++c) {
-            int cc = c8 * 16 + c;
-            float t = fq_s[cc] + bf2f(Qs[dd][cc]);
-            float tn = 1.f - 2.f * __builtin_amdgcn_rcpf(
-                __builtin_amdgcn_exp2f(2.f * LOG2E * t) + 1.f);
-            p = fmaf(tn, fo_s[cc], p);
-        }
-        p += __shfl_xor(p, 1); p += __shfl_xor(p, 2); p += __shfl_xor(p, 4);
-        if (c8 == 0) e_s[dd] = p + fbout[0];
-    }
-    __syncthreads();
-    if (tid < 64) {
-        float e = e_s[tid], mx = e;
-        for (int o = 32; o; o >>= 1) mx = fmaxf(mx, __shfl_xor(mx, o));
-        float pe = __expf(e - mx);
-        float s = pe;
-        for (int o = 32; o; o >>= 1) s += __shfl_xor(s, o);
-        e_s[tid] = pe / s;
-    }
-    __syncthreads();
-    if (tid < 256) {
-        int c2 = tid & 127, rg2 = tid >> 7;
-        float a = 0.f;
-        for (int d2 = rg2 * 32; d2 < rg2 * 32 + 32; ++d2)
-            a = fmaf(e_s[d2], bf2f(Ks[d2][c2]), a);
-        red_s[tid] = a;
-    }
-    __syncthreads();
-    if (tid < 128)
-        out[(size_t)b * 128 + tid] = red_s[tid] + red_s[tid + 128];
 }
 
 extern "C" void kernel_launch(void* const* d_in, const int* in_sizes, int n_in,
@@ -596,12 +621,16 @@
     const float* Fv = (const float*)d_in[26];  const float* fbv = (const float*)d_in[27];
     const float* Fout = (const float*)d_in[28]; const float* fbout = (const float*)d_in[29];
     float* out = (float*)d_out;
-    float* ws  = (float*)d_ws;
-
-    float* emb = ws;
-
-    gru_mfma_kernel<<<dim3(DD, BB / 32), 512, 0, stream>>>(x, mask, Wih, Whh, bih, bhh, emb);
-    tail_kernel<<<BB, 512, 0, stream>>>(
-        emb, Wq, bq, Wk, bk, Wv, bv, Wo, bo, W1, b1, W2, b2,
-        g1, be1, g2, be2, Fq, fbq, Fk, fbk, Fv, fbv, Fout, fbout, out);
-}
+    float* emb = (float*)d_ws;
+
+    void* kargs[] = {
+        (void*)&x, (void*)&mask, (void*)&Wih, (void*)&Whh, (void*)&bih, (void*)&bhh,
+        (void*)&Wq, (void*)&bq, (void*)&Wk, (void*)&bk, (void*)&Wv, (void*)&bv,
+        (void*)&Wo, (void*)&bo, (void*)&W1, (void*)&b1, (void*)&W2, (void*)&b2,
+        (void*)&g1, (void*)&be1, (void*)&g2, (void*)&be2,
+        (void*)&Fq, (void*)&fbq, (void*)&Fk, (void*)&fbk, (void*)&Fv, (void*)&fbv,
+        (void*)&Fout, (void*)&fbout, (void*)&emb, (void*)&out
+    };
+    hipLaunchCooperativeKernel((const void*)fused_kernel, dim3(256), dim3(512),
+                               kargs, 0, stream);
+}
```

After: 329.7 us. +43.7%, slower.
